# Kernel optimization log

Measured on AMD Instinct MI355X. Metric: run time of the kernel, lower is better.

Reference implementation:

```python
import jax, jax.numpy as jnp
import numpy as np

B, S, D, H = 4, 2048, 1024, 16
DH = D // H  # head dim = 64
MASK_VALUE = -1000000.0


def setup_inputs() -> dict:
    key = jax.random.key(0)
    ks = jax.random.split(key, 8)
    return {
        "key": jax.random.normal(ks[0], (B, S, D), jnp.float32),
        "query": jax.random.normal(ks[1], (B, S, D), jnp.float32),
        "value": jax.random.normal(ks[2], (B, S, D), jnp.float32),
        "valid_lens": jax.random.randint(ks[3], (B,), 0, 2048, jnp.int32),
        # nn.Linear weights stored as [out_features, in_features]
        "Wk": jax.random.normal(ks[4], (D, D), jnp.float32) / np.sqrt(D),
        "Wq": jax.random.normal(ks[5], (D, D), jnp.float32) / np.sqrt(D),
        "Wv": jax.random.normal(ks[6], (D, D), jnp.float32) / np.sqrt(D),
        "Wo": jax.random.normal(ks[7], (D, D), jnp.float32) / np.sqrt(D),
    }


def _split_heads(x):
    # [B, S, D] -> [B, H, S, DH]
    return x.reshape(B, S, H, DH).transpose(0, 2, 1, 3)


def reference(key, query, value, valid_lens, Wk, Wq, Wv, Wo):
    # projections (Linear: x @ W^T, bias=False)
    q = _split_heads(query @ Wq.T)  # [B, H, S, DH]
    k = _split_heads(key @ Wk.T)
    v = _split_heads(value @ Wv.T)

    scale = 1.0 / jnp.sqrt(jnp.asarray(DH, q.dtype))
    scores = jnp.einsum("bhqd,bhkd->bhqk", q, k) * scale  # [B, H, S, S]

    # valid_lens masks the key axis per batch element (same for all heads/queries)
    key_mask = jnp.arange(S) < valid_lens[:, None]  # [B, S]
    scores = jnp.where(key_mask[:, None, None, :], scores, MASK_VALUE)

    attn = jax.nn.softmax(scores, axis=-1)
    out = jnp.einsum("bhqk,bhkd->bhqd", attn, v)  # [B, H, S, DH]
    out = out.transpose(0, 2, 1, 3).reshape(B, S, D)  # concat heads
    return out @ Wo.T
```

## Files before the change

kernel.cpp:

```cpp
#include <hip/hip_runtime.h>
#include <hip/hip_bf16.h>
#include <stdint.h>

typedef __bf16 bf16;
typedef __bf16 bf16x4 __attribute__((ext_vector_type(4)));
typedef __bf16 bf16x8 __attribute__((ext_vector_type(8)));
typedef float f32x4 __attribute__((ext_vector_type(4)));
typedef float f32x8 __attribute__((ext_vector_type(8)));

#define MFMA16 __builtin_amdgcn_mfma_f32_16x16x32_bf16

__device__ __forceinline__ void gload_lds16(void* lds, const void* g) {
  __builtin_amdgcn_global_load_lds(
      (const __attribute__((address_space(1))) unsigned int*)g,
      (__attribute__((address_space(3))) unsigned int*)lds, 16, 0, 0);
}

#define S_BARRIER() __builtin_amdgcn_s_barrier()
#define WAIT_LGKM0()                                   \
  do {                                                 \
    asm volatile("s_waitcnt lgkmcnt(0)" ::: "memory"); \
    __builtin_amdgcn_sched_barrier(0);                 \
  } while (0)
#define WAIT_VM(n) asm volatile("s_waitcnt vmcnt(" #n ")" ::: "memory")

__global__ __launch_bounds__(256) void cvt3(
    const float* __restrict__ s0, const float* __restrict__ s1,
    const float* __restrict__ s2, bf16* __restrict__ d0,
    bf16* __restrict__ d1, bf16* __restrict__ d2) {
  const float* srcs[3] = {s0, s1, s2};
  bf16* dsts[3] = {d0, d1, d2};
  const float* src = srcs[blockIdx.y];
  bf16* dst = dsts[blockIdx.y];
  int i = (blockIdx.x * 256 + threadIdx.x) * 4;
  f32x4 v = *(const f32x4*)(src + i);
  bf16x4 o;
#pragma unroll
  for (int j = 0; j < 4; j++) o[j] = (bf16)v[j];
  *(bf16x4*)(dst + i) = o;
}

__global__ __launch_bounds__(256) void cvt1(const float* __restrict__ src,
                                            bf16* __restrict__ dst) {
  int i = (blockIdx.x * 256 + threadIdx.x) * 4;
  f32x4 v = *(const f32x4*)(src + i);
  bf16x4 o;
#pragma unroll
  for (int j = 0; j < 4; j++) o[j] = (bf16)v[j];
  *(bf16x4*)(dst + i) = o;
}

__global__ __launch_bounds__(256) void cvt4(const float* __restrict__ w0,
                                            const float* __restrict__ w1,
                                            const float* __restrict__ w2,
                                            const float* __restrict__ w3,
                                            bf16* __restrict__ dst) {
  const float* srcs[4] = {w0, w1, w2, w3};
  const float* src = srcs[blockIdx.y];
  int i = (blockIdx.x * 256 + threadIdx.x) * 4;
  f32x4 v = *(const f32x4*)(src + i);
  bf16x4 o;
#pragma unroll
  for (int j = 0; j < 4; j++) o[j] = (bf16)v[j];
  *(bf16x4*)(dst + (size_t)blockIdx.y * 1048576 + i) = o;
}

__device__ __forceinline__ void gemmF_body(const bf16* __restrict__ A,
                                           const bf16* __restrict__ W,
                                           void* __restrict__ Craw, int mode,
                                           int m0, int n0, bf16* smem) {
  constexpr int K = 1024;
  const int t = threadIdx.x;
  const int lane = t & 63;
  const int m16 = lane & 15;
  const int quad = (lane >> 4) & 3;
  const int sw = m16 & 7;
  const int w = t >> 6;
  const int wm = (w >> 2) * 64;
  const int wn = (w & 3) * 64;

  const bf16* Ab = A + (size_t)m0 * K;
  const bf16* Bb = W + (size_t)n0 * K;

  auto STG = [&](int buf, int kt) {
    bf16* dA = smem + buf * 24576;
    bf16* dB = dA + 8192;
    const bf16* sA = Ab + kt * 64;
    const bf16* sB = Bb + kt * 64;
#pragma unroll
    for (int ld = 0; ld < 2; ld++) {
      int idx = ld * 512 + t;
      int row = idx >> 3;
      int c = (idx & 7) ^ (row & 7);
      gload_lds16(dA + idx * 8, sA + (size_t)row * K + c * 8);
    }
#pragma unroll
    for (int ld = 0; ld < 4; ld++) {
      int idx = ld * 512 + t;
      int row = idx >> 3;
      int c = (idx & 7) ^ (row & 7);
      gload_lds16(dB + idx * 8, sB + (size_t)row * K + c * 8);
    }
  };

  bf16x8 aR[8], bR[8];
  auto LD = [&](int buf) {
    const bf16* As = smem + buf * 24576;
    const bf16* Bs = As + 8192;
#pragma unroll
    for (int f = 0; f < 4; f++)
#pragma unroll
      for (int ks = 0; ks < 2; ks++) {
        aR[f * 2 + ks] = *(const bf16x8*)&As[(wm + f * 16 + m16) * 64 +
                                             (((ks * 4 + quad) ^ sw) * 8)];
        bR[f * 2 + ks] = *(const bf16x8*)&Bs[(wn + f * 16 + m16) * 64 +
                                             (((ks * 4 + quad) ^ sw) * 8)];
      }
  };

  f32x4 acc[4][4];
#pragma unroll
  for (int f = 0; f < 4; f++)
#pragma unroll
    for (int g = 0; g < 4; g++) acc[f][g] = (f32x4){0.f, 0.f, 0.f, 0.f};

  auto MM = [&]() {
    __builtin_amdgcn_s_setprio(1);
#pragma unroll
    for (int f = 0; f < 4; f++)
#pragma unroll
      for (int g = 0; g < 4; g++)
#pragma unroll
        for (int ks = 0; ks < 2; ks++)
          acc[f][g] = MFMA16(aR[f * 2 + ks], bR[g * 2 + ks], acc[f][g], 0, 0, 0);
    __builtin_amdgcn_s_setprio(0);
  };

  STG(0, 0);
  STG(1, 1);
  WAIT_VM(6);
  S_BARRIER();

  int bufR = 0;
#pragma unroll 1
  for (int kt = 0; kt < 14; ++kt) {
    LD(bufR);
    int bufS = bufR + 2;
    if (bufS >= 3) bufS -= 3;
    STG(bufS, kt + 2);
    S_BARRIER();
    WAIT_LGKM0();
    MM();
    WAIT_VM(6);
    S_BARRIER();
    bufR = (bufR + 1 == 3) ? 0 : bufR + 1;
  }
  LD(bufR);
  S_BARRIER();
  WAIT_LGKM0();
  MM();
  WAIT_VM(0);
  S_BARRIER();
  bufR = (bufR + 1 == 3) ? 0 : bufR + 1;
  LD(bufR);
  S_BARRIER();
  WAIT_LGKM0();
  MM();

#pragma unroll
  for (int f = 0; f < 4; f++) {
    int rbase = m0 + wm + f * 16 + quad * 4;
#pragma unroll
    for (int g = 0; g < 4; g++) {
      int col = n0 + wn + g * 16 + m16;
#pragma unroll
      for (int r = 0; r < 4; r++) {
        int row = rbase + r;
        if (mode == 0) {
          ((float*)Craw)[(size_t)row * 1024 + col] = acc[f][g][r];
        } else {
          int b = row >> 11, s = row & 2047;
          int h = col >> 6, d = col & 63;
          bf16 v = (bf16)acc[f][g][r];
          if (mode == 1)
            ((bf16*)Craw)[(((size_t)(b * 16 + h)) * 2048 + s) * 64 + d] = v;
          else
            ((bf16*)Craw)[(((size_t)(b * 16 + h)) * 64 + d) * 2048 + s] = v;
        }
      }
    }
  }
}

__global__ __launch_bounds__(512, 2) void gemm_qkv(
    const bf16* __restrict__ xq, const bf16* __restrict__ xk,
    const bf16* __restrict__ xv, const bf16* __restrict__ wb,
    const int* __restrict__ vlen, bf16* __restrict__ qp,
    bf16* __restrict__ kp, bf16* __restrict__ vt) {
  __shared__ bf16 smem[73728];
  const int m0 = blockIdx.y * 128;
  const int n0 = blockIdx.x * 256;
  const int z = blockIdx.z;
  if (z >= 1) {
    int b = m0 >> 11;
    int s0 = m0 & 2047;
    int vl = vlen[b];
    if (vl != 0 && s0 >= vl) return;
  }
  const bf16* A = (z == 0) ? xq : (z == 1) ? xk : xv;
  const bf16* W = wb + (size_t)z * 1048576;
  bf16* C = (z == 0) ? qp : (z == 1) ? kp : vt;
  gemmF_body(A, W, C, (z == 2) ? 2 : 1, m0, n0, smem);
}

__global__ __launch_bounds__(512, 2) void gemm_one(const bf16* __restrict__ A,
                                                   const bf16* __restrict__ W,
                                                   void* __restrict__ Craw,
                                                   int mode) {
  __shared__ bf16 smem[73728];
  gemmF_body(A, W, Craw, mode, blockIdx.y * 128, blockIdx.x * 256, smem);
}

template <int AF32, int WF32>
__global__ __launch_bounds__(256) void gemm_bt(const void* __restrict__ Araw,
                                               const void* __restrict__ Wraw,
                                               void* __restrict__ Craw,
                                               int mode) {
  constexpr int K = 1024;
  __shared__ bf16 As[128 * 32];
  __shared__ bf16 Bs[128 * 32];
  const int t = threadIdx.x;
  const int lane = t & 63;
  const int quad = lane >> 4;
  const int m16 = lane & 15;
  const int w = t >> 6;
  const int m0 = blockIdx.y * 128;
  const int n0 = blockIdx.x * 128;
  const int wm = (w >> 1) * 64;
  const int wn = (w & 1) * 64;

  f32x4 acc[4][4];
#pragma unroll
  for (int i = 0; i < 4; i++)
#pragma unroll
    for (int j = 0; j < 4; j++) acc[i][j] = (f32x4){0.f, 0.f, 0.f, 0.f};

  for (int kt = 0; kt < K / 32; kt++) {
    bf16x8 aR[2], bR[2];
#pragma unroll
    for (int p = 0; p < 2; p++) {
      int idx = p * 256 + t;
      int row = idx >> 2;
      int ce = (idx & 3) * 8;
      size_t aoff = (size_t)(m0 + row) * K + kt * 32 + ce;
      size_t boff = (size_t)(n0 + row) * K + kt * 32 + ce;
      if constexpr (AF32) {
        f32x8 av = *(const f32x8*)((const float*)Araw + aoff);
#pragma unroll
        for (int j = 0; j < 8; j++) aR[p][j] = (bf16)av[j];
      } else {
        aR[p] = *(const bf16x8*)((const bf16*)Araw + aoff);
      }
      if constexpr (WF32) {
        f32x8 bv = *(const f32x8*)((const float*)Wraw + boff);
#pragma unroll
        for (int j = 0; j < 8; j++) bR[p][j] = (bf16)bv[j];
      } else {
        bR[p] = *(const bf16x8*)((const bf16*)Wraw + boff);
      }
    }
    __syncthreads();
#pragma unroll
    for (int p = 0; p < 2; p++) {
      int idx = p * 256 + t;
      *(bf16x8*)&As[idx * 8] = aR[p];
      *(bf16x8*)&Bs[idx * 8] = bR[p];
    }
    __syncthreads();

    bf16x8 af[4], bfr[4];
#pragma unroll
    for (int i = 0; i < 4; i++) {
      af[i] = *(const bf16x8*)&As[(wm + i * 16 + m16) * 32 + quad * 8];
      bfr[i] = *(const bf16x8*)&Bs[(wn + i * 16 + m16) * 32 + quad * 8];
    }
#pragma unroll
    for (int i = 0; i < 4; i++)
#pragma unroll
      for (int j = 0; j < 4; j++)
        acc[i][j] = MFMA16(af[i], bfr[j], acc[i][j], 0, 0, 0);
  }

#pragma unroll
  for (int i = 0; i < 4; i++) {
    int rbase = m0 + wm + i * 16 + quad * 4;
#pragma unroll
    for (int j = 0; j < 4; j++) {
      int col = n0 + wn + j * 16 + m16;
#pragma unroll
      for (int r = 0; r < 4; r++) {
        int row = rbase + r;
        if (mode == 0) {
          ((float*)Craw)[(size_t)row * 1024 + col] = acc[i][j][r];
        } else {
          int b = row >> 11, s = row & 2047;
          int h = col >> 6, d = col & 63;
          bf16 v = (bf16)acc[i][j][r];
          if (mode == 1)
            ((bf16*)Craw)[(((size_t)(b * 16 + h)) * 2048 + s) * 64 + d] = v;
          else
            ((bf16*)Craw)[(((size_t)(b * 16 + h)) * 64 + d) * 2048 + s] = v;
        }
      }
    }
  }
}

__global__ __launch_bounds__(512, 4) void attn(const bf16* __restrict__ qp,
                                               const bf16* __restrict__ kp,
                                               const bf16* __restrict__ vt,
                                               const int* __restrict__ vlen,
                                               bf16* __restrict__ ctx) {
  __shared__ bf16 Ks[2][4096];
  __shared__ bf16 Vs[2][4096];
  __shared__ bf16 Ps[8 * 2304];

  const int t = threadIdx.x;
  const int lane = t & 63;
  const int quad = (lane >> 4) & 3;
  const int m16 = lane & 15;
  const int sw = m16 & 7;
  const int w = t >> 6;
  const int id = blockIdx.y * 8 + blockIdx.x;
  const int xcd = id & 7;
  const int j = id >> 3;
  const int bh = (j >> 3) * 8 + xcd;
  const int qt = j & 7;
  const int b = bh >> 4;
  const int h = bh & 15;
  const int vl = vlen[b];

  const float C1 = 0.18033688f;
  const float C2 = 46.166241f;
  const float mArg = (vl == 0) ? 0.0f : -12800.0f;

  bf16x8 qf[2][2];
#pragma unroll
  for (int a = 0; a < 2; a++) {
    const bf16* qb =
        qp + ((size_t)(bh * 2048 + qt * 256 + w * 32 + a * 16 + m16)) * 64;
    qf[a][0] = *(const bf16x8*)(qb + quad * 8);
    qf[a][1] = *(const bf16x8*)(qb + 32 + quad * 8);
  }

  float rsum[2][4] = {{0.f, 0.f, 0.f, 0.f}, {0.f, 0.f, 0.f, 0.f}};
  f32x4 o[2][4];
#pragma unroll
  for (int a = 0; a < 2; a++)
#pragma unroll
    for (int nt = 0; nt < 4; nt++) o[a][nt] = (f32x4){0.f, 0.f, 0.f, 0.f};

  const int ktEnd = (vl == 0) ? 32 : ((vl + 63) >> 6);

  const int srow = t >> 3;
  const int sgc = (t & 7) ^ (srow & 7);
  auto STAGE = [&](int buf, int kt) {
    gload_lds16(&Ks[buf][t * 8],
                &kp[((size_t)(bh * 2048 + kt * 64 + srow)) * 64 + sgc * 8]);
    gload_lds16(&Vs[buf][t * 8],
                &vt[((size_t)(bh * 64 + srow)) * 2048 + kt * 64 + sgc * 8]);
  };

  STAGE(0, 0);

  for (int kt = 0; kt < ktEnd; kt++) {
    const int cur = kt & 1;
    if (kt + 1 < ktEnd) {
      STAGE(cur ^ 1, kt + 1);
      WAIT_VM(2);
    } else {
      WAIT_VM(0);
    }
    S_BARRIER();
    const bf16* Ksb = Ks[cur];
    const bf16* Vsb = Vs[cur];

    f32x4 s[2][4];
#pragma unroll
    for (int a = 0; a < 2; a++)
#pragma unroll
      for (int nt = 0; nt < 4; nt++) s[a][nt] = (f32x4){0.f, 0.f, 0.f, 0.f};
#pragma unroll
    for (int nt = 0; nt < 4; nt++) {
      int key = nt * 16 + m16;
#pragma unroll
      for (int ks = 0; ks < 2; ks++) {
        bf16x8 kf =
            *(const bf16x8*)&Ksb[key * 64 + (((ks * 4 + quad) ^ sw) * 8)];
        s[0][nt] = MFMA16(qf[0][ks], kf, s[0][nt], 0, 0, 0);
        s[1][nt] = MFMA16(qf[1][ks], kf, s[1][nt], 0, 0, 0);
      }
    }

#pragma unroll
    for (int nt = 0; nt < 4; nt++) {
      bool masked = (kt * 64 + nt * 16 + m16) >= vl;
#pragma unroll
      for (int a = 0; a < 2; a++)
#pragma unroll
        for (int r = 0; r < 4; r++) {
          float arg = masked ? mArg : (s[a][nt][r] * C1 - C2);
          bf16 pb = (bf16)__builtin_amdgcn_exp2f(arg);
          rsum[a][r] += (float)pb;
          Ps[w * 2304 + (a * 16 + quad * 4 + r) * 72 + nt * 16 + m16] = pb;
        }
    }

#pragma unroll
    for (int ks = 0; ks < 2; ks++) {
      bf16x8 pf0 = *(const bf16x8*)&Ps[w * 2304 + m16 * 72 + ks * 32 + quad * 8];
      bf16x8 pf1 =
          *(const bf16x8*)&Ps[w * 2304 + (16 + m16) * 72 + ks * 32 + quad * 8];
#pragma unroll
      for (int nt = 0; nt < 4; nt++) {
        int dh = nt * 16 + m16;
        bf16x8 vf =
            *(const bf16x8*)&Vsb[dh * 64 + (((ks * 4 + quad) ^ sw) * 8)];
        o[0][nt] = MFMA16(pf0, vf, o[0][nt], 0, 0, 0);
        o[1][nt] = MFMA16(pf1, vf, o[1][nt], 0, 0, 0);
      }
    }
    S_BARRIER();
  }

#pragma unroll
  for (int off = 1; off < 16; off <<= 1)
#pragma unroll
    for (int a = 0; a < 2; a++)
#pragma unroll
      for (int r = 0; r < 4; r++) rsum[a][r] += __shfl_xor(rsum[a][r], off);
#pragma unroll
  for (int a = 0; a < 2; a++)
#pragma unroll
    for (int r = 0; r < 4; r++) rsum[a][r] = 1.0f / rsum[a][r];

#pragma unroll
  for (int a = 0; a < 2; a++)
#pragma unroll
    for (int nt = 0; nt < 4; nt++) {
      int dh = nt * 16 + m16;
#pragma unroll
      for (int r = 0; r < 4; r++) {
        int sr = qt * 256 + w * 32 + a * 16 + quad * 4 + r;
        ctx[((size_t)(b * 2048 + sr)) * 1024 + h * 64 + dh] =
            (bf16)(o[a][nt][r] * rsum[a][r]);
      }
    }
}

extern "C" void kernel_launch(void* const* d_in, const int* in_sizes, int n_in,
                              void* d_out, int out_size, void* d_ws,
                              size_t ws_size, hipStream_t stream) {
  const float* key = (const float*)d_in[0];
  const float* query = (const float*)d_in[1];
  const float* value = (const float*)d_in[2];
  const int* vlen = (const int*)d_in[3];
  const float* Wk = (const float*)d_in[4];
  const float* Wq = (const float*)d_in[5];
  const float* Wv = (const float*)d_in[6];
  const float* Wo = (const float*)d_in[7];

  const size_t NE = (size_t)4 * 2048 * 1024;
  const size_t WE = 1048576;

  const size_t needA = (6 * NE + 4 * WE) * sizeof(bf16);
  const size_t needB = (5 * NE + 4 * WE) * sizeof(bf16);
  dim3 gg(4, 64), gb(512), cb(256), ag(8, 64), ab(512);

  if (ws_size >= needA) {
    bf16* qp = (bf16*)d_ws;
    bf16* kp = qp + NE;
    bf16* vt = kp + NE;
    bf16* xq = vt + NE;
    bf16* xk = xq + NE;
    bf16* xv = xk + NE;
    bf16* wb = xv + NE;
    bf16* ctx = xq;

    cvt4<<<dim3(1024, 4), cb, 0, stream>>>(Wq, Wk, Wv, Wo, wb);
    cvt3<<<dim3(8192, 3), cb, 0, stream>>>(query, key, value, xq, xk, xv);
    gemm_qkv<<<dim3(4, 64, 3), gb, 0, stream>>>(xq, xk, xv, wb, vlen, qp, kp,
                                                vt);
    attn<<<ag, ab, 0, stream>>>(qp, kp, vt, vlen, ctx);
    gemm_one<<<gg, gb, 0, stream>>>(ctx, wb + 3 * WE, d_out, 0);
  } else if (ws_size >= needB) {
    bf16* qp = (bf16*)d_ws;
    bf16* kp = qp + NE;
    bf16* vt = kp + NE;
    bf16* ctx = vt + NE;
    bf16* xb = ctx + NE;
    bf16* wb = xb + NE;

    cvt4<<<dim3(1024, 4), cb, 0, stream>>>(Wq, Wk, Wv, Wo, wb);
    cvt1<<<8192, cb, 0, stream>>>(query, xb);
    gemm_one<<<gg, gb, 0, stream>>>(xb, wb + 0 * WE, qp, 1);
    cvt1<<<8192, cb, 0, stream>>>(key, xb);
    gemm_one<<<gg, gb, 0, stream>>>(xb, wb + 1 * WE, kp, 1);
    cvt1<<<8192, cb, 0, stream>>>(value, xb);
    gemm_one<<<gg, gb, 0, stream>>>(xb, wb + 2 * WE, vt, 2);
    attn<<<ag, ab, 0, stream>>>(qp, kp, vt, vlen, ctx);
    gemm_one<<<gg, gb, 0, stream>>>(ctx, wb + 3 * WE, d_out, 0);
  } else {
    bf16* qp = (bf16*)d_ws;
    bf16* kp = qp + NE;
    bf16* vt = kp + NE;
    bf16* ctx = vt + NE;
    dim3 g8(8, 64), b256(256);
    gemm_bt<1, 1><<<g8, b256, 0, stream>>>(query, Wq, qp, 1);
    gemm_bt<1, 1><<<g8, b256, 0, stream>>>(key, Wk, kp, 1);
    gemm_bt<1, 1><<<g8, b256, 0, stream>>>(value, Wv, vt, 2);
    attn<<<ag, ab, 0, stream>>>(qp, kp, vt, vlen, ctx);
    gemm_bt<0, 1><<<g8, b256, 0, stream>>>(ctx, Wo, d_out, 0);
  }
}
```

Baseline: 328.7 us.

## Keep softmax probabilities in registers via transposed QK MFMA and permuted V staging

Swaps the MFMA operand order so the score tile comes out transposed, which lets the exponentiated probabilities be packed straight into bf16x8 A-operands for the PV MFMA. This removes the per-wave LDS round trip for P and its shared buffer. V is now staged with 4-byte global-to-LDS loads whose key order is permuted to match the new P register layout. Masking is applied only on the boundary tile, and the row-sum reduction shrinks to two cross-lane shuffles. The cost is four times as many small V loads per stage and more complex address arithmetic.

```diff
diff --git a/kernel.cpp b/kernel.cpp
--- a/kernel.cpp
+++ b/kernel.cpp
@@ -15,8 +15,14 @@
       (const __attribute__((address_space(1))) unsigned int*)g,
       (__attribute__((address_space(3))) unsigned int*)lds, 16, 0, 0);
 }
+__device__ __forceinline__ void gload_lds4(void* lds, const void* g) {
+  __builtin_amdgcn_global_load_lds(
+      (const __attribute__((address_space(1))) unsigned int*)g,
+      (__attribute__((address_space(3))) unsigned int*)lds, 4, 0, 0);
+}
 
 #define S_BARRIER() __builtin_amdgcn_s_barrier()
+#define SCHED_FENCE() __builtin_amdgcn_sched_barrier(0)
 #define WAIT_LGKM0()                                   \
   do {                                                 \
     asm volatile("s_waitcnt lgkmcnt(0)" ::: "memory"); \
@@ -323,7 +329,6 @@
                                                bf16* __restrict__ ctx) {
   __shared__ bf16 Ks[2][4096];
   __shared__ bf16 Vs[2][4096];
-  __shared__ bf16 Ps[8 * 2304];
 
   const int t = threadIdx.x;
   const int lane = t & 63;
@@ -342,7 +347,8 @@
 
   const float C1 = 0.18033688f;
   const float C2 = 46.166241f;
-  const float mArg = (vl == 0) ? 0.0f : -12800.0f;
+  const float sC1 = (vl == 0) ? 0.0f : C1;
+  const float sC2 = (vl == 0) ? 0.0f : C2;
 
   bf16x8 qf[2][2];
 #pragma unroll
@@ -353,7 +359,7 @@
     qf[a][1] = *(const bf16x8*)(qb + 32 + quad * 8);
   }
 
-  float rsum[2][4] = {{0.f, 0.f, 0.f, 0.f}, {0.f, 0.f, 0.f, 0.f}};
+  float rsum[2] = {0.f, 0.f};
   f32x4 o[2][4];
 #pragma unroll
   for (int a = 0; a < 2; a++)
@@ -362,13 +368,26 @@
 
   const int ktEnd = (vl == 0) ? 32 : ((vl + 63) >> 6);
 
-  const int srow = t >> 3;
-  const int sgc = (t & 7) ^ (srow & 7);
-  auto STAGE = [&](int buf, int kt) {
+  const int krow = t >> 3;
+  const int kgc = (t & 7) ^ (krow & 7);
+  auto STAGE = [&](int buf, int kt2) {
     gload_lds16(&Ks[buf][t * 8],
-                &kp[((size_t)(bh * 2048 + kt * 64 + srow)) * 64 + sgc * 8]);
-    gload_lds16(&Vs[buf][t * 8],
-                &vt[((size_t)(bh * 64 + srow)) * 2048 + kt * 64 + sgc * 8]);
+                &kp[((size_t)(bh * 2048 + kt2 * 64 + krow)) * 64 + kgc * 8]);
+#pragma unroll
+    for (int ld = 0; ld < 4; ld++) {
+      int c = ld * 512 + t;
+      int dh = c >> 5;
+      int i4 = c & 31;
+      int c8 = i4 >> 2;
+      int jw = i4 & 3;
+      int lc = c8 ^ (dh & 7);
+      int slot = lc * 8 + jw * 2;
+      int ks2 = slot >> 5;
+      int w32 = slot & 31;
+      int key = ks2 * 32 + ((w32 >> 2) & 1) * 16 + (w32 >> 3) * 4 + (w32 & 3);
+      gload_lds4(&Vs[buf][c * 2],
+                 &vt[((size_t)(bh * 64 + dh)) * 2048 + kt2 * 64 + key]);
+    }
   };
 
   STAGE(0, 0);
@@ -377,11 +396,12 @@
     const int cur = kt & 1;
     if (kt + 1 < ktEnd) {
       STAGE(cur ^ 1, kt + 1);
-      WAIT_VM(2);
+      WAIT_VM(5);
     } else {
       WAIT_VM(0);
     }
     S_BARRIER();
+    SCHED_FENCE();
     const bf16* Ksb = Ks[cur];
     const bf16* Vsb = Vs[cur];
 
@@ -392,70 +412,82 @@
       for (int nt = 0; nt < 4; nt++) s[a][nt] = (f32x4){0.f, 0.f, 0.f, 0.f};
 #pragma unroll
     for (int nt = 0; nt < 4; nt++) {
-      int key = nt * 16 + m16;
 #pragma unroll
       for (int ks = 0; ks < 2; ks++) {
-        bf16x8 kf =
-            *(const bf16x8*)&Ksb[key * 64 + (((ks * 4 + quad) ^ sw) * 8)];
-        s[0][nt] = MFMA16(qf[0][ks], kf, s[0][nt], 0, 0, 0);
-        s[1][nt] = MFMA16(qf[1][ks], kf, s[1][nt], 0, 0, 0);
-      }
-    }
-
-#pragma unroll
-    for (int nt = 0; nt < 4; nt++) {
-      bool masked = (kt * 64 + nt * 16 + m16) >= vl;
+        bf16x8 kf = *(const bf16x8*)&Ksb[(nt * 16 + m16) * 64 +
+                                         (((ks * 4 + quad) ^ sw) * 8)];
+        s[0][nt] = MFMA16(kf, qf[0][ks], s[0][nt], 0, 0, 0);
+        s[1][nt] = MFMA16(kf, qf[1][ks], s[1][nt], 0, 0, 0);
+      }
+    }
+
+    bf16x8 pa[2][2];
+    const bool partial = (vl != 0) && (kt == (vl >> 6));
+    if (!partial) {
 #pragma unroll
       for (int a = 0; a < 2; a++)
 #pragma unroll
-        for (int r = 0; r < 4; r++) {
-          float arg = masked ? mArg : (s[a][nt][r] * C1 - C2);
-          bf16 pb = (bf16)__builtin_amdgcn_exp2f(arg);
-          rsum[a][r] += (float)pb;
-          Ps[w * 2304 + (a * 16 + quad * 4 + r) * 72 + nt * 16 + m16] = pb;
+        for (int nt = 0; nt < 4; nt++)
+#pragma unroll
+          for (int r = 0; r < 4; r++) {
+            float p = __builtin_amdgcn_exp2f(s[a][nt][r] * sC1 - sC2);
+            bf16 pb = (bf16)p;
+            rsum[a] += (float)pb;
+            pa[a][nt >> 1][(nt & 1) * 4 + r] = pb;
+          }
+    } else {
+#pragma unroll
+      for (int a = 0; a < 2; a++)
+#pragma unroll
+        for (int nt = 0; nt < 4; nt++) {
+          int keyb = kt * 64 + nt * 16 + quad * 4;
+#pragma unroll
+          for (int r = 0; r < 4; r++) {
+            float arg = (keyb + r >= vl) ? -12800.0f
+                                         : (s[a][nt][r] * sC1 - sC2);
+            float p = __builtin_amdgcn_exp2f(arg);
+            bf16 pb = (bf16)p;
+            rsum[a] += (float)pb;
+            pa[a][nt >> 1][(nt & 1) * 4 + r] = pb;
+          }
         }
     }
 
 #pragma unroll
     for (int ks = 0; ks < 2; ks++) {
-      bf16x8 pf0 = *(const bf16x8*)&Ps[w * 2304 + m16 * 72 + ks * 32 + quad * 8];
-      bf16x8 pf1 =
-          *(const bf16x8*)&Ps[w * 2304 + (16 + m16) * 72 + ks * 32 + quad * 8];
+#pragma unroll
+      for (int nt = 0; nt < 4; nt++) {
+        bf16x8 vf = *(const bf16x8*)&Vsb[(nt * 16 + m16) * 64 +
+                                         (((ks * 4 + quad) ^ sw) * 8)];
+        o[0][nt] = MFMA16(pa[0][ks], vf, o[0][nt], 0, 0, 0);
+        o[1][nt] = MFMA16(pa[1][ks], vf, o[1][nt], 0, 0, 0);
+      }
+    }
+    S_BARRIER();
+    SCHED_FENCE();
+  }
+
+#pragma unroll
+  for (int a = 0; a < 2; a++) {
+    rsum[a] += __shfl_xor(rsum[a], 16);
+    rsum[a] += __shfl_xor(rsum[a], 32);
+    rsum[a] = 1.0f / rsum[a];
+  }
+
+#pragma unroll
+  for (int a = 0; a < 2; a++) {
+#pragma unroll
+    for (int r = 0; r < 4; r++) {
+      float rr = __shfl(rsum[a], (lane & 48) | (quad * 4 + r));
 #pragma unroll
       for (int nt = 0; nt < 4; nt++) {
         int dh = nt * 16 + m16;
-        bf16x8 vf =
-            *(const bf16x8*)&Vsb[dh * 64 + (((ks * 4 + quad) ^ sw) * 8)];
-        o[0][nt] = MFMA16(pf0, vf, o[0][nt], 0, 0, 0);
-        o[1][nt] = MFMA16(pf1, vf, o[1][nt], 0, 0, 0);
-      }
-    }
-    S_BARRIER();
-  }
-
-#pragma unroll
-  for (int off = 1; off < 16; off <<= 1)
-#pragma unroll
-    for (int a = 0; a < 2; a++)
-#pragma unroll
-      for (int r = 0; r < 4; r++) rsum[a][r] += __shfl_xor(rsum[a][r], off);
-#pragma unroll
-  for (int a = 0; a < 2; a++)
-#pragma unroll
-    for (int r = 0; r < 4; r++) rsum[a][r] = 1.0f / rsum[a][r];
-
-#pragma unroll
-  for (int a = 0; a < 2; a++)
-#pragma unroll
-    for (int nt = 0; nt < 4; nt++) {
-      int dh = nt * 16 + m16;
-#pragma unroll
-      for (int r = 0; r < 4; r++) {
         int sr = qt * 256 + w * 32 + a * 16 + quad * 4 + r;
         ctx[((size_t)(b * 2048 + sr)) * 1024 + h * 64 + dh] =
-            (bf16)(o[a][nt][r] * rsum[a][r]);
-      }
-    }
+            (bf16)(o[a][nt][r] * rr);
+      }
+    }
+  }
 }
 
 extern "C" void kernel_launch(void* const* d_in, const int* in_sizes, int n_in,
```

Result: slower. 367.7 us (+11.9%).
